# Kernel tuning notes

Measured on AMD Instinct MI355X. Metric: run time of the kernel, lower is better.

## Reference

```python
import jax, jax.numpy as jnp
import numpy as np

K_SIZE, STRIDE, PAD = 3, 2, 1

def _conv1x1(x, w, b):
    return jnp.einsum('bchw,oc->bohw', x, w) + b[None, :, None, None]

def _unfold(x, k, s, p):
    # Matches torch F.unfold ordering: channel-major, then (kh, kw). -> [B, C, k*k, L]
    B, C, H, W = x.shape
    xp = jnp.pad(x, ((0, 0), (0, 0), (p, p), (p, p)))
    ho = (H + 2 * p - k) // s + 1
    wo = (W + 2 * p - k) // s + 1
    cols = []
    for i in range(k):
        for j in range(k):
            cols.append(xp[:, :, i:i + s * (ho - 1) + 1:s, j:j + s * (wo - 1) + 1:s])
    patches = jnp.stack(cols, axis=2)            # [B, C, k*k, ho, wo]
    return patches.reshape(B, C, k * k, ho * wo)

def _forward(shallow, deep, K_w, K_b, KSA_w, KSA_b):
    B, C, H, W = shallow.shape
    d = (2 * C) // 16
    h, w = H // STRIDE, W // STRIDE
    hw = h * w
    max_out = _conv1x1(deep, KSA_w, KSA_b)            # [B, d, h, w]
    # global re-score branch
    max_out1 = jnp.max(max_out, axis=1)               # [B, h, w]
    q = max_out1.reshape(B, hw)                       # [B, hw]
    kt = max_out.reshape(B, hw, d)                    # faithful to torch .view(B,-1,d) (channel-scrambled flat view)
    lit = jnp.einsum('bp,bpd->bd', q, kt) / hw        # mean over hw of outer products -> [B, d]
    V = max_out.reshape(B, d, hw)
    re_score = jnp.einsum('bd,bdp->bp', lit, V).reshape(B, 1, h, w)
    sig = jax.nn.sigmoid(re_score)
    # local windowed attention branch
    Kx = _conv1x1(shallow, K_w, K_b)                  # [B, out, H, W]
    Kunf = _unfold(Kx, K_SIZE, STRIDE, PAD)           # [B, out, kk, hw]
    # torch does matmul([d,1],[1,kk]) then mean over d == mean_d(q_d) * K patch element
    qmean = jnp.mean(max_out, axis=1).reshape(B, 1, 1, hw)
    logits = qmean * Kunf                             # [B, out, kk, hw]
    new_kernel = jax.nn.softmax(logits, axis=2)       # softmax over window dim kk
    att = jnp.sum(new_kernel * Kunf, axis=2)          # [B, out, hw]
    att = att.reshape(B, -1, h, w)
    return sig * att + att, re_score

def setup_inputs():
    key = jax.random.key(0)
    ks = jax.random.split(key, 6)
    B, C, H, W = 4, 256, 128, 128
    out_c, d = 256, (2 * C) // 16
    return {
        'shallow': jax.random.normal(ks[0], (B, C, H, W), jnp.float32),
        'deep': jax.random.normal(ks[1], (B, 2 * C, H // 2, W // 2), jnp.float32),
        'K_w': jax.random.normal(ks[2], (out_c, C), jnp.float32) * 0.02,
        'K_b': jax.random.normal(ks[3], (out_c,), jnp.float32) * 0.02,
        'KSA_w': jax.random.normal(ks[4], (d, 2 * C), jnp.float32) * 0.02,
        'KSA_b': jax.random.normal(ks[5], (d,), jnp.float32) * 0.02,
    }

def reference(shallow, deep, K_w, K_b, KSA_w, KSA_b):
    return _forward(shallow, deep, K_w, K_b, KSA_w, KSA_b)
```

## Files before the change

### kernel.cpp

```cpp
#include <hip/hip_runtime.h>

typedef unsigned short u16;
typedef __attribute__((ext_vector_type(8))) short short8;
typedef __attribute__((ext_vector_type(4))) float float4v;
typedef __attribute__((ext_vector_type(4))) unsigned short ushort4v;

__device__ __forceinline__ u16 f2bf(float f) {
    unsigned u = __float_as_uint(f);
    u += 0x7FFFu + ((u >> 16) & 1u);
    return (u16)(u >> 16);
}
__device__ __forceinline__ float bf2f(u16 u) {
    return __uint_as_float(((unsigned)u) << 16);
}

__device__ float g_maxout[4 * 32 * 4096];
__device__ float g_q[16384];
__device__ float g_qmean[16384];
__device__ float g_lit[128];
__device__ float g_sigfac[16384];
__device__ u16   g_Kw_bf[65536];
__device__ u16   g_KSAw_bf[16384];
__device__ u16   g_Kx[4 * 256 * 16384];

__global__ __launch_bounds__(256) void prep_kernel(
    const float* __restrict__ Kw, const float* __restrict__ KSAw)
{
    const int idx = blockIdx.x * 256 + threadIdx.x;
    if (idx < 128) g_lit[idx] = 0.f;
    if (idx < 65536) g_Kw_bf[idx] = f2bf(Kw[idx]);
    if (idx < 16384) g_KSAw_bf[idx] = f2bf(KSAw[idx]);
}

__global__ __launch_bounds__(256) void gemm_deep(
    const float* __restrict__ Bias, const float* __restrict__ X)
{
    __shared__ u16 As[16384];
    const int t = threadIdx.x;
    const int wave = t >> 6, lane = t & 63;
    const int quad = lane >> 4, n16 = lane & 15;
    const int b = blockIdx.y;
    const int p = blockIdx.x * 64 + wave * 16 + n16;
    const float* Xb = X + ((long long)b << 21) + p;

#pragma unroll
    for (int c = 0; c < 8; c++) {
        const int idx = (c << 8) + t;
        *(short8*)(As + idx * 8) = *(const short8*)(g_KSAw_bf + idx * 8);
    }

    float breg[2][8];
#pragma unroll
    for (int j = 0; j < 8; j++) breg[0][j] = Xb[((quad << 3) + j) << 12];
#pragma unroll
    for (int j = 0; j < 8; j++) breg[1][j] = Xb[(32 + (quad << 3) + j) << 12];

    __syncthreads();

    float4v acc[2];
#pragma unroll
    for (int i = 0; i < 2; i++) acc[i] = (float4v){0.f, 0.f, 0.f, 0.f};

#pragma unroll
    for (int kb = 0; kb < 16; kb++) {
        const int cur = kb & 1;
        short8 bfrag;
#pragma unroll
        for (int j = 0; j < 8; j++) bfrag[j] = (short)f2bf(breg[cur][j]);
        if (kb < 14) {
            const float* xp = Xb + (((kb + 2) << 5) << 12);
#pragma unroll
            for (int j = 0; j < 8; j++) breg[cur][j] = xp[((quad << 3) + j) << 12];
        }
        const u16* ap = As + n16 * 512 + kb * 32 + quad * 8;
#pragma unroll
        for (int ot = 0; ot < 2; ot++) {
            const short8 afrag = *(const short8*)(ap + ot * 8192);
            acc[ot] = __builtin_amdgcn_mfma_f32_16x16x32_bf16(afrag, bfrag, acc[ot], 0, 0, 0);
        }
    }

    float mx = -3.4e38f, sm = 0.f;
#pragma unroll
    for (int ot = 0; ot < 2; ot++) {
#pragma unroll
        for (int r = 0; r < 4; r++) {
            const int o = ot * 16 + quad * 4 + r;
            const float v = acc[ot][r] + Bias[o];
            g_maxout[((b * 32 + o) << 12) + p] = v;
            mx = fmaxf(mx, v);
            sm += v;
        }
    }
    mx = fmaxf(mx, __shfl_xor(mx, 16, 64));
    sm += __shfl_xor(sm, 16, 64);
    mx = fmaxf(mx, __shfl_xor(mx, 32, 64));
    sm += __shfl_xor(sm, 32, 64);
    if (quad == 0) {
        g_q[(b << 12) + p] = mx;
        g_qmean[(b << 12) + p] = sm * (1.f / 32.f);
    }
}

__global__ __launch_bounds__(256) void lit_kernel()
{
    const int b = blockIdx.y;
    const int f0 = blockIdx.x * 8192;
    const int t = threadIdx.x;
    const float* mo = g_maxout + (b << 17);
    const float* qb = g_q + (b << 12);
    float acc = 0.f;
#pragma unroll
    for (int it = 0; it < 32; it++) {
        const int f = f0 + it * 256 + t;
        acc += qb[f >> 5] * mo[f];
    }
    __shared__ float red[256];
    red[t] = acc;
    __syncthreads();
    if (t < 32) {
        float s = 0.f;
#pragma unroll
        for (int k = 0; k < 8; k++) s += red[t + k * 32];
        atomicAdd(&g_lit[b * 32 + t], s * (1.f / 4096.f));
    }
}

__global__ __launch_bounds__(256) void rescore_kernel(float* __restrict__ out_re)
{
    const int idx = blockIdx.x * 256 + threadIdx.x;
    const int b = idx >> 12, p = idx & 4095;
    const float* mo = g_maxout + (b << 17) + p;
    const float* lb = g_lit + b * 32;
    float r = 0.f;
#pragma unroll
    for (int j = 0; j < 32; j++) r += lb[j] * mo[j << 12];
    out_re[idx] = r;
    g_sigfac[idx] = 1.f + 1.f / (1.f + __expf(-r));
}

__global__ __launch_bounds__(256) void gemm_kx(
    const float* __restrict__ Bias, const float* __restrict__ X)
{
    __shared__ u16 Bs[4][2048];
    const int t = threadIdx.x;
    const int wave = t >> 6, lane = t & 63;
    const int quad = lane >> 4, n16 = lane & 15;
    const int b = blockIdx.y;
    const int p0 = blockIdx.x * 64;
    const float* Xb = X + ((long long)b << 22) + p0 + wave * 16 + n16;
    const u16* Ab = g_Kw_bf + (wave * 64 + n16) * 256 + quad * 8;
    const int cxor = (n16 >> 1) & 3;
    const int swz = (quad ^ cxor) << 3;
    const int bwr = (wave * 16 + n16) * 32 + swz;

    float4v acc[4][4];
#pragma unroll
    for (int i = 0; i < 4; i++)
#pragma unroll
        for (int j = 0; j < 4; j++) acc[i][j] = (float4v){0.f, 0.f, 0.f, 0.f};

    short8 areg[2][4];
    float breg[2][8];

#define BLOAD(dst, kb_) \
    _Pragma("unroll") for (int j = 0; j < 8; j++) \
        dst[j] = Xb[(((kb_) << 5) + (quad << 3) + j) << 14];
#define ALOAD(dst, kb_) \
    _Pragma("unroll") for (int ot = 0; ot < 4; ot++) \
        dst[ot] = *(const short8*)(Ab + ot * 4096 + ((kb_) << 5));
#define BSTORE(src, kb_) { \
    short8 w_; \
    _Pragma("unroll") for (int j = 0; j < 8; j++) w_[j] = (short)f2bf(src[j]); \
    *(short8*)(&Bs[(kb_) & 3][bwr]) = w_; }

    BLOAD(breg[0], 0)
    BLOAD(breg[1], 1)
    ALOAD(areg[0], 0)
    BSTORE(breg[0], 0)
    BSTORE(breg[1], 1)
    BLOAD(breg[0], 2)
    __syncthreads();

#pragma unroll
    for (int kb = 0; kb < 8; kb++) {
        const int cr = kb & 1;
        if (kb < 7) ALOAD(areg[cr ^ 1], kb + 1)
        if (kb + 3 < 8) BLOAD(breg[cr ^ 1], kb + 3)
#pragma unroll
        for (int cg = 0; cg < 4; cg++) {
            const short8 bfrag = *(const short8*)(&Bs[kb & 3][(cg * 16 + n16) * 32 + swz]);
#pragma unroll
            for (int ot = 0; ot < 4; ot++)
                acc[ot][cg] = __builtin_amdgcn_mfma_f32_16x16x32_bf16(
                    bfrag, areg[cr][ot], acc[ot][cg], 0, 0, 0);
        }
        if (kb + 2 < 8) BSTORE(breg[cr], kb + 2)
        __syncthreads();
    }
#undef BLOAD
#undef ALOAD
#undef BSTORE

    u16* kxb = g_Kx + (((long long)b << 8) << 14);
#pragma unroll
    for (int ot = 0; ot < 4; ot++) {
        const int o = wave * 64 + ot * 16 + n16;
        const float bo = Bias[o];
        u16* orow = kxb + ((long long)o << 14) + p0 + quad * 4;
#pragma unroll
        for (int cg = 0; cg < 4; cg++) {
            ushort4v w;
#pragma unroll
            for (int r = 0; r < 4; r++) w[r] = f2bf(acc[ot][cg][r] + bo);
            *(ushort4v*)(orow + cg * 16) = w;
        }
    }
}

__global__ __launch_bounds__(256) void att_window(float* __restrict__ out)
{
    __shared__ float tile[9][130];
    const int t = threadIdx.x;
    const int o = blockIdx.y, b = blockIdx.z;
    const int y0 = (blockIdx.x << 3) - 1;
    const u16* kxp = g_Kx + ((((long long)b << 8) + o) << 14);

    if (t < 9) tile[t][64] = 0.f;
#pragma unroll
    for (int k = 0; k < 5; k++) {
        const int e = (k << 8) + t;
        if (e < 1152) {
            const int r = e >> 7, x = e & 127;
            const int y = y0 + r;
            const float val = (y >= 0 && y < 128) ? bf2f(kxp[(y << 7) + x]) : 0.f;
            const int slot = (x & 1) ? (65 + (x >> 1)) : (x >> 1);
            tile[r][slot] = val;
        }
    }
    __syncthreads();

    const int p = (blockIdx.x << 8) + t;
    const int pw = t & 63;
    const int rl = (t >> 6) << 1;
    const float m = g_qmean[(b << 12) + p];
    const float sf = g_sigfac[(b << 12) + p];

    float v[9];
#pragma unroll
    for (int ki = 0; ki < 3; ++ki) {
        v[ki * 3 + 0] = tile[rl + ki][64 + pw];
        v[ki * 3 + 1] = tile[rl + ki][pw];
        v[ki * 3 + 2] = tile[rl + ki][65 + pw];
    }

    float mx = -3.4e38f;
#pragma unroll
    for (int k = 0; k < 9; ++k) mx = fmaxf(mx, m * v[k]);
    float s = 0.f, a = 0.f;
#pragma unroll
    for (int k = 0; k < 9; ++k) {
        const float e = __expf(m * v[k] - mx);
        s += e;
        a += e * v[k];
    }
    out[((((long long)b << 8) + o) << 12) + p] = (a / s) * sf;
}

extern "C" void kernel_launch(void* const* d_in, const int* in_sizes, int n_in,
                              void* d_out, int out_size, void* d_ws, size_t ws_size,
                              hipStream_t stream) {
    const float *shallow = 0, *deep = 0, *K_w = 0, *K_b = 0, *KSA_w = 0, *KSA_b = 0;
    for (int i = 0; i < n_in; ++i) {
        switch (in_sizes[i]) {
            case 16777216: shallow = (const float*)d_in[i]; break;
            case 8388608:  deep    = (const float*)d_in[i]; break;
            case 65536:    K_w     = (const float*)d_in[i]; break;
            case 256:      K_b     = (const float*)d_in[i]; break;
            case 16384:    KSA_w   = (const float*)d_in[i]; break;
            case 32:       KSA_b   = (const float*)d_in[i]; break;
        }
    }
    float* out = (float*)d_out;

    prep_kernel<<<320, 256, 0, stream>>>(K_w, KSA_w);
    gemm_deep<<<dim3(64, 4), 256, 0, stream>>>(KSA_b, deep);
    lit_kernel<<<dim3(16, 4), 256, 0, stream>>>();
    rescore_kernel<<<64, 256, 0, stream>>>(out + 4194304);
    gemm_kx<<<dim3(256, 4), 256, 0, stream>>>(K_b, shallow);
    att_window<<<dim3(16, 256, 4), 256, 0, stream>>>(out);
}
```

Baseline: 190.3 us.

## Keep packed K weights in registers for gemm_kx and batch channels in att_window

Repacks K_w into MFMA fragment order in the prep kernel so gemm_kx can hold all A fragments in registers. It then streams X directly from global memory into MFMA operands without shared-memory staging or barriers. att_window is changed to process 8 output channels per block with packed 32-bit bf16 loads, reducing block count and per-block overhead. The trade-off is much higher register pressure in gemm_kx and a larger shared tile in att_window.

```diff
diff --git a/kernel.cpp b/kernel.cpp
--- a/kernel.cpp
+++ b/kernel.cpp
@@ -19,7 +19,7 @@
 __device__ float g_qmean[16384];
 __device__ float g_lit[128];
 __device__ float g_sigfac[16384];
-__device__ u16   g_Kw_bf[65536];
+__device__ u16   g_KwP[65536];
 __device__ u16   g_KSAw_bf[16384];
 __device__ u16   g_Kx[4 * 256 * 16384];
 
@@ -28,7 +28,12 @@
 {
     const int idx = blockIdx.x * 256 + threadIdx.x;
     if (idx < 128) g_lit[idx] = 0.f;
-    if (idx < 65536) g_Kw_bf[idx] = f2bf(Kw[idx]);
+    if (idx < 65536) {
+        const int o = idx >> 8, c = idx & 255;
+        const int fi = ((o >> 4) << 3) + (c >> 5);
+        const int lane = (((c >> 3) & 3) << 4) + (o & 15);
+        g_KwP[((fi << 6) + lane) * 8 + (c & 7)] = f2bf(Kw[idx]);
+    }
     if (idx < 16384) g_KSAw_bf[idx] = f2bf(KSAw[idx]);
 }
 
@@ -139,20 +144,23 @@
     g_sigfac[idx] = 1.f + 1.f / (1.f + __expf(-r));
 }
 
-__global__ __launch_bounds__(256) void gemm_kx(
+__global__ __launch_bounds__(256, 2) void gemm_kx(
     const float* __restrict__ Bias, const float* __restrict__ X)
 {
-    __shared__ u16 Bs[4][2048];
     const int t = threadIdx.x;
     const int wave = t >> 6, lane = t & 63;
     const int quad = lane >> 4, n16 = lane & 15;
     const int b = blockIdx.y;
     const int p0 = blockIdx.x * 64;
-    const float* Xb = X + ((long long)b << 22) + p0 + wave * 16 + n16;
-    const u16* Ab = g_Kw_bf + (wave * 64 + n16) * 256 + quad * 8;
-    const int cxor = (n16 >> 1) & 3;
-    const int swz = (quad ^ cxor) << 3;
-    const int bwr = (wave * 16 + n16) * 32 + swz;
+    const float* Xb = X + ((long long)b << 22) + p0;
+
+    short8 af[4][8];
+    const short8* Ap = (const short8*)g_KwP + ((wave * 4) << 3) * 64 + lane;
+#pragma unroll
+    for (int ot = 0; ot < 4; ot++)
+#pragma unroll
+        for (int kb = 0; kb < 8; kb++)
+            af[ot][kb] = Ap[(((ot << 3) + kb) << 6)];
 
     float4v acc[4][4];
 #pragma unroll
@@ -160,83 +168,64 @@
 #pragma unroll
         for (int j = 0; j < 4; j++) acc[i][j] = (float4v){0.f, 0.f, 0.f, 0.f};
 
-    short8 areg[2][4];
-    float breg[2][8];
-
-#define BLOAD(dst, kb_) \
-    _Pragma("unroll") for (int j = 0; j < 8; j++) \
-        dst[j] = Xb[(((kb_) << 5) + (quad << 3) + j) << 14];
-#define ALOAD(dst, kb_) \
-    _Pragma("unroll") for (int ot = 0; ot < 4; ot++) \
-        dst[ot] = *(const short8*)(Ab + ot * 4096 + ((kb_) << 5));
-#define BSTORE(src, kb_) { \
-    short8 w_; \
-    _Pragma("unroll") for (int j = 0; j < 8; j++) w_[j] = (short)f2bf(src[j]); \
-    *(short8*)(&Bs[(kb_) & 3][bwr]) = w_; }
-
-    BLOAD(breg[0], 0)
-    BLOAD(breg[1], 1)
-    ALOAD(areg[0], 0)
-    BSTORE(breg[0], 0)
-    BSTORE(breg[1], 1)
-    BLOAD(breg[0], 2)
-    __syncthreads();
-
-#pragma unroll
-    for (int kb = 0; kb < 8; kb++) {
-        const int cr = kb & 1;
-        if (kb < 7) ALOAD(areg[cr ^ 1], kb + 1)
-        if (kb + 3 < 8) BLOAD(breg[cr ^ 1], kb + 3)
-#pragma unroll
-        for (int cg = 0; cg < 4; cg++) {
-            const short8 bfrag = *(const short8*)(&Bs[kb & 3][(cg * 16 + n16) * 32 + swz]);
-#pragma unroll
-            for (int ot = 0; ot < 4; ot++)
-                acc[ot][cg] = __builtin_amdgcn_mfma_f32_16x16x32_bf16(
-                    bfrag, areg[cr][ot], acc[ot][cg], 0, 0, 0);
-        }
-        if (kb + 2 < 8) BSTORE(breg[cr], kb + 2)
-        __syncthreads();
-    }
-#undef BLOAD
-#undef ALOAD
-#undef BSTORE
+    float xr[3][8];
+#define XLOAD(dst, s_) { \
+    const int kb_ = (s_) >> 2, pg_ = (s_) & 3; \
+    const float* xp_ = Xb + (((kb_ << 5) + (quad << 3)) << 14) + (pg_ << 4) + n16; \
+    _Pragma("unroll") for (int j = 0; j < 8; j++) dst[j] = xp_[j << 14]; }
+
+    XLOAD(xr[0], 0)
+    XLOAD(xr[1], 1)
+#pragma unroll
+    for (int s = 0; s < 32; s++) {
+        if (s < 30) XLOAD(xr[(s + 2) % 3], s + 2)
+        short8 bx;
+#pragma unroll
+        for (int j = 0; j < 8; j++) bx[j] = (short)f2bf(xr[s % 3][j]);
+        const int kb = s >> 2, pg = s & 3;
+#pragma unroll
+        for (int ot = 0; ot < 4; ot++)
+            acc[pg][ot] = __builtin_amdgcn_mfma_f32_16x16x32_bf16(
+                bx, af[ot][kb], acc[pg][ot], 0, 0, 0);
+    }
+#undef XLOAD
 
     u16* kxb = g_Kx + (((long long)b << 8) << 14);
 #pragma unroll
     for (int ot = 0; ot < 4; ot++) {
         const int o = wave * 64 + ot * 16 + n16;
         const float bo = Bias[o];
-        u16* orow = kxb + ((long long)o << 14) + p0 + quad * 4;
-#pragma unroll
-        for (int cg = 0; cg < 4; cg++) {
+        u16* orow = kxb + ((long long)o << 14) + p0 + (quad << 2);
+#pragma unroll
+        for (int pg = 0; pg < 4; pg++) {
             ushort4v w;
 #pragma unroll
-            for (int r = 0; r < 4; r++) w[r] = f2bf(acc[ot][cg][r] + bo);
-            *(ushort4v*)(orow + cg * 16) = w;
+            for (int r = 0; r < 4; r++) w[r] = f2bf(acc[pg][ot][r] + bo);
+            *(ushort4v*)(orow + (pg << 4)) = w;
         }
     }
 }
 
 __global__ __launch_bounds__(256) void att_window(float* __restrict__ out)
 {
-    __shared__ float tile[9][130];
-    const int t = threadIdx.x;
-    const int o = blockIdx.y, b = blockIdx.z;
+    __shared__ float tile[8][9][130];
+    const int t = threadIdx.x;
+    const int o0 = blockIdx.y << 3, b = blockIdx.z;
     const int y0 = (blockIdx.x << 3) - 1;
-    const u16* kxp = g_Kx + ((((long long)b << 8) + o) << 14);
-
-    if (t < 9) tile[t][64] = 0.f;
-#pragma unroll
-    for (int k = 0; k < 5; k++) {
+    const u16* kxb = g_Kx + (((long long)b << 8) << 14);
+
+    if (t < 72) tile[t / 9][t % 9][64] = 0.f;
+#pragma unroll
+    for (int k = 0; k < 18; k++) {
         const int e = (k << 8) + t;
-        if (e < 1152) {
-            const int r = e >> 7, x = e & 127;
-            const int y = y0 + r;
-            const float val = (y >= 0 && y < 128) ? bf2f(kxp[(y << 7) + x]) : 0.f;
-            const int slot = (x & 1) ? (65 + (x >> 1)) : (x >> 1);
-            tile[r][slot] = val;
-        }
+        const int row = e >> 6, pr = e & 63;
+        const int oi = row / 9, r = row - oi * 9;
+        const int y = y0 + r;
+        unsigned v = 0;
+        if (y >= 0 && y < 128)
+            v = *(const unsigned*)(kxb + (((long long)(o0 + oi)) << 14) + (y << 7) + (pr << 1));
+        tile[oi][r][pr] = bf2f((u16)(v & 0xffffu));
+        tile[oi][r][65 + pr] = bf2f((u16)(v >> 16));
     }
     __syncthreads();
 
@@ -246,25 +235,27 @@
     const float m = g_qmean[(b << 12) + p];
     const float sf = g_sigfac[(b << 12) + p];
 
-    float v[9];
-#pragma unroll
-    for (int ki = 0; ki < 3; ++ki) {
-        v[ki * 3 + 0] = tile[rl + ki][64 + pw];
-        v[ki * 3 + 1] = tile[rl + ki][pw];
-        v[ki * 3 + 2] = tile[rl + ki][65 + pw];
-    }
-
-    float mx = -3.4e38f;
-#pragma unroll
-    for (int k = 0; k < 9; ++k) mx = fmaxf(mx, m * v[k]);
-    float s = 0.f, a = 0.f;
-#pragma unroll
-    for (int k = 0; k < 9; ++k) {
-        const float e = __expf(m * v[k] - mx);
-        s += e;
-        a += e * v[k];
-    }
-    out[((((long long)b << 8) + o) << 12) + p] = (a / s) * sf;
+#pragma unroll
+    for (int oi = 0; oi < 8; oi++) {
+        float v[9];
+#pragma unroll
+        for (int ki = 0; ki < 3; ++ki) {
+            v[ki * 3 + 0] = tile[oi][rl + ki][64 + pw];
+            v[ki * 3 + 1] = tile[oi][rl + ki][pw];
+            v[ki * 3 + 2] = tile[oi][rl + ki][65 + pw];
+        }
+        float mx = -3.4e38f;
+#pragma unroll
+        for (int k = 0; k < 9; ++k) mx = fmaxf(mx, m * v[k]);
+        float s = 0.f, a = 0.f;
+#pragma unroll
+        for (int k = 0; k < 9; ++k) {
+            const float e = __expf(m * v[k] - mx);
+            s += e;
+            a += e * v[k];
+        }
+        out[((((long long)b << 8) + o0 + oi) << 12) + p] = (a / s) * sf;
+    }
 }
 
 extern "C" void kernel_launch(void* const* d_in, const int* in_sizes, int n_in,
@@ -288,5 +279,5 @@
     lit_kernel<<<dim3(16, 4), 256, 0, stream>>>();
     rescore_kernel<<<64, 256, 0, stream>>>(out + 4194304);
     gemm_kx<<<dim3(256, 4), 256, 0, stream>>>(K_b, shallow);
-    att_window<<<dim3(16, 256, 4), 256, 0, stream>>>(out);
-}
+    att_window<<<dim3(16, 32, 4), 256, 0, stream>>>(out);
+}
```

Result: slower. 225.7 us (+18.6%).
